# Optimization experiments

Measured on AMD Instinct MI355X. Metric: run time of the kernel, lower is better.

## Reference

```python
import jax, jax.numpy as jnp
import numpy as np

B, M, N = 32, 256, 4000          # images, gt boxes/img, proposals/img
NUM_CLASSES = 80                 # cfg.MODEL.ROI_HEADS.NUM_CLASSES
BATCH_PER_IMG = 512              # cfg.MODEL.ROI_HEADS.BATCH_SIZE_PER_IMAGE
POS_FRAC = 0.25                  # cfg.MODEL.ROI_HEADS.POSITIVE_FRACTION
IOU_THRESH = 0.5                 # cfg.MODEL.ROI_HEADS.IOU_THRESHOLDS
IMG_SIZE = 1024.0


def _make_boxes(key, shape):
    # valid xyxy boxes: centers in [0, IMG_SIZE], sides in [4, 256]
    k1, k2 = jax.random.split(key)
    c = jax.random.uniform(k1, shape[:-1] + (2,)) * IMG_SIZE
    wh = 4.0 + jax.random.uniform(k2, shape[:-1] + (2,)) * 252.0
    return jnp.concatenate([c - wh / 2, c + wh / 2], axis=-1)


def setup_inputs() -> dict:
    key = jax.random.key(0)
    kg, kp, kc, kr = jax.random.split(key, 4)
    gt_boxes = _make_boxes(kg, (B, M, 4))
    proposal_boxes = _make_boxes(kp, (B, N, 4))
    gt_classes = jax.random.randint(kc, (B, M), 0, NUM_CLASSES, dtype=jnp.int32)
    # random priorities stand in for torch.randperm in subsample_labels
    rand_priority = jax.random.uniform(kr, (B, N + M))
    return {"gt_boxes": gt_boxes, "proposal_boxes": proposal_boxes,
            "gt_classes": gt_classes, "rand_priority": rand_priority}


def _pairwise_iou(b1, b2):
    # b1 [M,4], b2 [K,4] -> [M,K]  (detectron2 pairwise_iou)
    a1 = (b1[:, 2] - b1[:, 0]) * (b1[:, 3] - b1[:, 1])
    a2 = (b2[:, 2] - b2[:, 0]) * (b2[:, 3] - b2[:, 1])
    lt = jnp.maximum(b1[:, None, :2], b2[None, :, :2])
    rb = jnp.minimum(b1[:, None, 2:], b2[None, :, 2:])
    wh = jnp.clip(rb - lt, 0.0)
    inter = wh[..., 0] * wh[..., 1]
    union = a1[:, None] + a2[None, :] - inter
    return jnp.where(inter > 0, inter / union, 0.0)


def _rank_desc(score):
    # rank of each element in descending order of score
    order = jnp.argsort(-score)
    return jnp.zeros_like(order).at[order].set(jnp.arange(order.shape[0]))


def _per_image(gt_b, prop_b, gt_c, pri):
    # add_ground_truth_to_proposals (proposal_append_gt=True)
    boxes = jnp.concatenate([prop_b, gt_b], axis=0)          # [N+M, 4]
    iou = _pairwise_iou(gt_b, boxes)                          # [M, N+M]
    # Matcher(thresholds=[0.5], labels=[0,1], allow_low_quality=False)
    matched_idxs = jnp.argmax(iou, axis=0)                    # [N+M]
    matched_vals = jnp.max(iou, axis=0)
    matched_labels = (matched_vals >= IOU_THRESH).astype(jnp.int32)
    # _sample_proposals: assign classes, bg where label==0
    cls = gt_c[matched_idxs]
    cls = jnp.where(matched_labels == 0, NUM_CLASSES, cls)
    # subsample_labels with random priorities (fixed-shape, jit-safe)
    fg = cls < NUM_CLASSES
    bg = cls == NUM_CLASSES
    num_fg = jnp.minimum(fg.sum(), int(BATCH_PER_IMG * POS_FRAC))
    num_bg = jnp.minimum(bg.sum(), BATCH_PER_IMG - num_fg)
    sel_fg = fg & (_rank_desc(jnp.where(fg, pri, -jnp.inf)) < num_fg)
    sel_bg = bg & (_rank_desc(jnp.where(bg, pri, -jnp.inf)) < num_bg)
    sel = sel_fg | sel_bg
    _, idx = jax.lax.top_k(jnp.where(sel, pri, -jnp.inf), BATCH_PER_IMG)
    labels = jnp.where(sel[idx], cls[idx], -1)                # pad -1 if <512 valid
    return iou, matched_idxs, matched_labels, idx, labels


def reference(gt_boxes, proposal_boxes, gt_classes, rand_priority):
    return jax.vmap(_per_image)(gt_boxes, proposal_boxes, gt_classes, rand_priority)
```

## Files before the change

kernel.cpp:

```cpp
#include <hip/hip_runtime.h>
#include <hip/hip_bf16.h>

#define Bimg 32
#define Mgt 256
#define Nprop 4000
#define KBOX (Nprop + Mgt)
#define NCLS 80
#define BATCH 512
#define NFG_CAP 128
#define NBINS 1024
#define BINCAP 1024
#define MT 32
#define MS (Mgt / MT)
#define KCH ((KBOX + 1023) / 1024)

typedef float f32x4 __attribute__((ext_vector_type(4)));

__global__ __launch_bounds__(256) void iou_part_kernel(
    const float* __restrict__ gt_boxes,
    const float* __restrict__ prop_boxes,
    float* __restrict__ out_iou,
    unsigned long long* __restrict__ part)
{
    const int b  = blockIdx.z;
    const int ms = blockIdx.y;
    const int m0 = ms * MT;
    const int k0 = (blockIdx.x * 256 + threadIdx.x) * 4;

    __shared__ float4 gbox[MT];
    __shared__ float  garea[MT];
    if (threadIdx.x < MT) {
        float4 g = ((const float4*)(gt_boxes + (size_t)b * Mgt * 4))[m0 + threadIdx.x];
        gbox[threadIdx.x] = g;
        garea[threadIdx.x] = (g.z - g.x) * (g.w - g.y);
    }
    __syncthreads();
    if (k0 >= KBOX) return;

    float4 bx[4]; float a2[4];
    if (k0 < Nprop) {
        const float4* pp = (const float4*)(prop_boxes + (size_t)b * Nprop * 4);
        #pragma unroll
        for (int c = 0; c < 4; ++c) bx[c] = pp[k0 + c];
    } else {
        const float4* gg = (const float4*)(gt_boxes + (size_t)b * Mgt * 4);
        #pragma unroll
        for (int c = 0; c < 4; ++c) bx[c] = gg[k0 - Nprop + c];
    }
    #pragma unroll
    for (int c = 0; c < 4; ++c) a2[c] = (bx[c].z - bx[c].x) * (bx[c].w - bx[c].y);

    unsigned long long bk[4] = {0ull, 0ull, 0ull, 0ull};
    float* orow = out_iou + (size_t)b * Mgt * KBOX + (size_t)m0 * KBOX + k0;

    for (int mm = 0; mm < MT; ++mm) {
        float4 g = gbox[mm];
        float ga = garea[mm];
        float io[4];
        #pragma unroll
        for (int c = 0; c < 4; ++c) {
            float ltx = fmaxf(g.x, bx[c].x), lty = fmaxf(g.y, bx[c].y);
            float rbx = fminf(g.z, bx[c].z), rby = fminf(g.w, bx[c].w);
            float w = fmaxf(rbx - ltx, 0.0f);
            float h = fmaxf(rby - lty, 0.0f);
            float inter = w * h;
            float uni = ga + a2[c] - inter;
            float iou = (inter > 0.0f) ? (inter / uni) : 0.0f;
            io[c] = iou;
            unsigned long long key =
                ((unsigned long long)__float_as_uint(iou) << 8) |
                (unsigned long long)(255 - (m0 + mm));
            if (key > bk[c]) bk[c] = key;
        }
        f32x4 res = { io[0], io[1], io[2], io[3] };
        __builtin_nontemporal_store(res, (f32x4*)(orow + (size_t)mm * KBOX));
    }

    unsigned long long* pr = part + ((size_t)b * MS + ms) * KBOX + k0;
    *(ulonglong2*)(pr)     = make_ulonglong2(bk[0], bk[1]);
    *(ulonglong2*)(pr + 2) = make_ulonglong2(bk[2], bk[3]);
}

__global__ __launch_bounds__(256) void match_reduce_kernel(
    const unsigned long long* __restrict__ part,
    float* __restrict__ out_midx,
    float* __restrict__ out_mlab)
{
    const int b = blockIdx.y;
    const int k = blockIdx.x * 256 + threadIdx.x;
    if (k >= KBOX) return;
    unsigned long long best = 0ull;
    #pragma unroll
    for (int s = 0; s < MS; ++s) {
        unsigned long long key = part[((size_t)b * MS + s) * KBOX + k];
        if (key > best) best = key;
    }
    float v = __uint_as_float((unsigned)(best >> 8));
    int   m = 255 - (int)(best & 0xFFull);
    out_midx[(size_t)b * KBOX + k] = (float)m;
    out_mlab[(size_t)b * KBOX + k] = (v >= 0.5f) ? 1.0f : 0.0f;
}

__global__ __launch_bounds__(1024) void sample_kernel(
    const int*   __restrict__ gt_classes,
    const float* __restrict__ pri,
    const float* __restrict__ midx,
    const float* __restrict__ mlab,
    float* __restrict__ out_idx,
    float* __restrict__ out_lab)
{
    const int b   = blockIdx.x;
    const int tid = threadIdx.x;

    __shared__ unsigned long long keys[KBOX];
    __shared__ unsigned short     clsS[KBOX];
    __shared__ unsigned char      selA[KBOX];
    __shared__ int histP[NBINS];
    __shared__ int sufP[NBINS];
    __shared__ unsigned long long binFG[BINCAP];
    __shared__ unsigned long long binBG[BINCAP];
    __shared__ unsigned long long selKeys[BATCH];
    __shared__ int cntF, cntB, cntSel, sTF, sTB;

    histP[tid] = 0;
    if (tid == 0) { cntF = 0; cntB = 0; cntSel = 0; sTF = -1; sTB = -1; }
    __syncthreads();

    for (int i = tid; i < KBOX; i += 1024) {
        float p  = pri[(size_t)b * KBOX + i];
        int   mi = (int)midx[(size_t)b * KBOX + i];
        float ml = mlab[(size_t)b * KBOX + i];
        int c = (ml != 0.0f) ? gt_classes[b * Mgt + mi] : NCLS;
        clsS[i] = (unsigned short)c;
        selA[i] = 0;
        unsigned pb = __float_as_uint(p);
        keys[i] = ((unsigned long long)pb << 32) |
                  (unsigned long long)(0xFFFFFFFFu - (unsigned)i);
        int bucket = (int)(p * (float)NBINS);
        bucket = min(max(bucket, 0), NBINS - 1);
        atomicAdd(&histP[bucket], (c < NCLS) ? 1 : (1 << 16));
    }
    __syncthreads();

    sufP[tid] = histP[tid];
    __syncthreads();
    for (int off = 1; off < NBINS; off <<= 1) {
        int v = sufP[tid];
        int add = (tid + off < NBINS) ? sufP[tid + off] : 0;
        __syncthreads();
        sufP[tid] = v + add;
        __syncthreads();
    }
    const int total_fg = sufP[0] & 0xFFFF;
    const int total_bg = (sufP[0] >> 16) & 0xFFFF;
    const int num_fg = min(total_fg, NFG_CAP);
    const int num_bg = min(total_bg, BATCH - num_fg);

    {
        int sf  = sufP[tid] & 0xFFFF;
        int sfn = (tid < NBINS - 1) ? (sufP[tid + 1] & 0xFFFF) : 0;
        if (num_fg > 0 && sf >= num_fg && sfn < num_fg) sTF = tid;
        int sb  = (sufP[tid] >> 16) & 0xFFFF;
        int sbn = (tid < NBINS - 1) ? ((sufP[tid + 1] >> 16) & 0xFFFF) : 0;
        if (num_bg > 0 && sb >= num_bg && sbn < num_bg) sTB = tid;
    }
    __syncthreads();
    const int tF = sTF, tB = sTB;
    const int aboveF = (tF >= 0 && tF < NBINS - 1) ? (sufP[tF + 1] & 0xFFFF) : 0;
    const int aboveB = (tB >= 0 && tB < NBINS - 1) ? ((sufP[tB + 1] >> 16) & 0xFFFF) : 0;
    const int needF = num_fg - aboveF;
    const int needB = num_bg - aboveB;

    for (int i = tid; i < KBOX; i += 1024) {
        unsigned long long key = keys[i];
        float p = __uint_as_float((unsigned)(key >> 32));
        int bucket = (int)(p * (float)NBINS);
        bucket = min(max(bucket, 0), NBINS - 1);
        if (clsS[i] < NCLS) {
            if (tF >= 0) {
                if (bucket > tF) selA[i] = 1;
                else if (bucket == tF) { int j = atomicAdd(&cntF, 1); if (j < BINCAP) binFG[j] = key; }
            }
        } else {
            if (tB >= 0) {
                if (bucket > tB) selA[i] = 1;
                else if (bucket == tB) { int j = atomicAdd(&cntB, 1); if (j < BINCAP) binBG[j] = key; }
            }
        }
    }
    __syncthreads();

    {
        int cf = min(cntF, BINCAP);
        for (int j = tid; j < cf; j += 1024) {
            unsigned long long key = binFG[j];
            int rank = 0;
            for (int l = 0; l < cf; ++l) rank += (binFG[l] > key) ? 1 : 0;
            if (rank < needF) { unsigned kk = 0xFFFFFFFFu - (unsigned)(key & 0xFFFFFFFFull); selA[kk] = 1; }
        }
        int cb = min(cntB, BINCAP);
        for (int j = tid; j < cb; j += 1024) {
            unsigned long long key = binBG[j];
            int rank = 0;
            for (int l = 0; l < cb; ++l) rank += (binBG[l] > key) ? 1 : 0;
            if (rank < needB) { unsigned kk = 0xFFFFFFFFu - (unsigned)(key & 0xFFFFFFFFull); selA[kk] = 1; }
        }
    }
    __syncthreads();

    const int total_sel = num_fg + num_bg;
    if (tid < BATCH && tid >= total_sel) selKeys[tid] = 0ull;
    for (int i = tid; i < KBOX; i += 1024) {
        if (selA[i]) {
            int p = atomicAdd(&cntSel, 1);
            selKeys[p] = keys[i];
        }
    }
    __syncthreads();

    for (int k2 = 2; k2 <= BATCH; k2 <<= 1) {
        for (int j = k2 >> 1; j > 0; j >>= 1) {
            if (tid < BATCH) {
                int i = tid, ixj = i ^ j;
                if (ixj > i) {
                    unsigned long long a = selKeys[i], c2 = selKeys[ixj];
                    bool up = ((i & k2) == 0);
                    if (up ? (a < c2) : (a > c2)) { selKeys[i] = c2; selKeys[ixj] = a; }
                }
            }
            __syncthreads();
        }
    }

    if (tid < BATCH) {
        unsigned long long key = selKeys[tid];
        if (key != 0ull) {
            unsigned kk = 0xFFFFFFFFu - (unsigned)(key & 0xFFFFFFFFull);
            out_idx[b * BATCH + tid] = (float)kk;
            out_lab[b * BATCH + tid] = (float)clsS[kk];
        }
    }

    if (total_sel < BATCH) {
        __syncthreads();
        int loc[5]; int acc = 0;
        #pragma unroll
        for (int q = 0; q < 5; ++q) {
            int i = tid * 5 + q;
            int contrib = (i < KBOX && !selA[i]) ? 1 : 0;
            loc[q] = acc; acc += contrib;
        }
        histP[tid] = acc;
        __syncthreads();
        for (int off = 1; off < 1024; off <<= 1) {
            int v = histP[tid];
            int add = (tid >= off) ? histP[tid - off] : 0;
            __syncthreads();
            histP[tid] = v + add;
            __syncthreads();
        }
        int excl = tid ? histP[tid - 1] : 0;
        #pragma unroll
        for (int q = 0; q < 5; ++q) {
            int i = tid * 5 + q;
            if (i < KBOX && !selA[i]) {
                int p = total_sel + excl + loc[q];
                if (p < BATCH) { out_idx[b * BATCH + p] = (float)i; out_lab[b * BATCH + p] = -1.0f; }
            }
        }
    }
}

extern "C" void kernel_launch(void* const* d_in, const int* in_sizes, int n_in,
                              void* d_out, int out_size, void* d_ws, size_t ws_size,
                              hipStream_t stream) {
    const float* gt_boxes   = (const float*)d_in[0];
    const float* prop_boxes = (const float*)d_in[1];
    const int*   gt_classes = (const int*)d_in[2];
    const float* rand_pri   = (const float*)d_in[3];

    float* out = (float*)d_out;
    const size_t off_iou  = 0;
    const size_t off_midx = (size_t)Bimg * Mgt * KBOX;
    const size_t off_mlab = off_midx + (size_t)Bimg * KBOX;
    const size_t off_idx  = off_mlab + (size_t)Bimg * KBOX;
    const size_t off_lab  = off_idx  + (size_t)Bimg * BATCH;

    unsigned long long* part = (unsigned long long*)d_ws;

    dim3 gridA(KCH, MS, Bimg);
    iou_part_kernel<<<gridA, 256, 0, stream>>>(
        gt_boxes, prop_boxes, out + off_iou, part);

    dim3 gridR((KBOX + 255) / 256, Bimg);
    match_reduce_kernel<<<gridR, 256, 0, stream>>>(
        part, out + off_midx, out + off_mlab);

    sample_kernel<<<Bimg, 1024, 0, stream>>>(
        gt_classes, rand_pri,
        out + off_midx, out + off_mlab,
        out + off_idx, out + off_lab);
}
```

Before: 65.89 us.

## Fuse match reduction via atomicMax, replace bitonic sort with rank scatter, warp-shuffle scan

The separate match-reduce kernel is removed. The IoU kernel now does a global 64-bit atomicMax of packed (iou, gt index) keys into a zeroed buffer, and the sampling kernel decodes matched index and label itself. The GT tile shrinks from 32 to 16 rows, which doubles the grid. The sampling kernel packs the class into the priority key, replaces the suffix-sum loop with wave-shuffle scans, and replaces the 512-element bitonic sort with an O(n^2) rank-and-scatter. The change trades one kernel launch and the partials round trip for a memset and atomic contention.

```diff
diff --git a/kernel.cpp b/kernel.cpp
--- a/kernel.cpp
+++ b/kernel.cpp
@@ -10,17 +10,18 @@
 #define NFG_CAP 128
 #define NBINS 1024
 #define BINCAP 1024
-#define MT 32
+#define MT 16
 #define MS (Mgt / MT)
 #define KCH ((KBOX + 1023) / 1024)
 
 typedef float f32x4 __attribute__((ext_vector_type(4)));
+typedef unsigned long long ull;
 
 __global__ __launch_bounds__(256) void iou_part_kernel(
     const float* __restrict__ gt_boxes,
     const float* __restrict__ prop_boxes,
     float* __restrict__ out_iou,
-    unsigned long long* __restrict__ part)
+    ull* __restrict__ gpart)
 {
     const int b  = blockIdx.z;
     const int ms = blockIdx.y;
@@ -50,7 +51,8 @@
     #pragma unroll
     for (int c = 0; c < 4; ++c) a2[c] = (bx[c].z - bx[c].x) * (bx[c].w - bx[c].y);
 
-    unsigned long long bk[4] = {0ull, 0ull, 0ull, 0ull};
+    float bestv[4] = {-1.f, -1.f, -1.f, -1.f};
+    int   bestm[4] = {0, 0, 0, 0};
     float* orow = out_iou + (size_t)b * Mgt * KBOX + (size_t)m0 * KBOX + k0;
 
     for (int mm = 0; mm < MT; ++mm) {
@@ -67,59 +69,43 @@
             float uni = ga + a2[c] - inter;
             float iou = (inter > 0.0f) ? (inter / uni) : 0.0f;
             io[c] = iou;
-            unsigned long long key =
-                ((unsigned long long)__float_as_uint(iou) << 8) |
-                (unsigned long long)(255 - (m0 + mm));
-            if (key > bk[c]) bk[c] = key;
+            if (iou > bestv[c]) { bestv[c] = iou; bestm[c] = m0 + mm; }
         }
         f32x4 res = { io[0], io[1], io[2], io[3] };
         __builtin_nontemporal_store(res, (f32x4*)(orow + (size_t)mm * KBOX));
     }
 
-    unsigned long long* pr = part + ((size_t)b * MS + ms) * KBOX + k0;
-    *(ulonglong2*)(pr)     = make_ulonglong2(bk[0], bk[1]);
-    *(ulonglong2*)(pr + 2) = make_ulonglong2(bk[2], bk[3]);
-}
-
-__global__ __launch_bounds__(256) void match_reduce_kernel(
-    const unsigned long long* __restrict__ part,
-    float* __restrict__ out_midx,
-    float* __restrict__ out_mlab)
-{
-    const int b = blockIdx.y;
-    const int k = blockIdx.x * 256 + threadIdx.x;
-    if (k >= KBOX) return;
-    unsigned long long best = 0ull;
+    ull* pr = gpart + (size_t)b * KBOX + k0;
     #pragma unroll
-    for (int s = 0; s < MS; ++s) {
-        unsigned long long key = part[((size_t)b * MS + s) * KBOX + k];
-        if (key > best) best = key;
-    }
-    float v = __uint_as_float((unsigned)(best >> 8));
-    int   m = 255 - (int)(best & 0xFFull);
-    out_midx[(size_t)b * KBOX + k] = (float)m;
-    out_mlab[(size_t)b * KBOX + k] = (v >= 0.5f) ? 1.0f : 0.0f;
+    for (int c = 0; c < 4; ++c) {
+        ull key = ((ull)__float_as_uint(bestv[c]) << 8) |
+                  (ull)(255 - bestm[c]);
+        atomicMax(pr + c, key);
+    }
 }
 
 __global__ __launch_bounds__(1024) void sample_kernel(
     const int*   __restrict__ gt_classes,
     const float* __restrict__ pri,
-    const float* __restrict__ midx,
-    const float* __restrict__ mlab,
+    const ull*   __restrict__ gpart,
+    float* __restrict__ out_midx,
+    float* __restrict__ out_mlab,
     float* __restrict__ out_idx,
     float* __restrict__ out_lab)
 {
-    const int b   = blockIdx.x;
-    const int tid = threadIdx.x;
-
-    __shared__ unsigned long long keys[KBOX];
-    __shared__ unsigned short     clsS[KBOX];
-    __shared__ unsigned char      selA[KBOX];
+    const int b    = blockIdx.x;
+    const int tid  = threadIdx.x;
+    const int lane = tid & 63;
+    const int wv   = tid >> 6;
+
+    __shared__ ull keys[KBOX];
+    __shared__ unsigned char selA[KBOX];
     __shared__ int histP[NBINS];
-    __shared__ int sufP[NBINS];
-    __shared__ unsigned long long binFG[BINCAP];
-    __shared__ unsigned long long binBG[BINCAP];
-    __shared__ unsigned long long selKeys[BATCH];
+    __shared__ int sufP[NBINS + 1];
+    __shared__ ull binFG[BINCAP];
+    __shared__ ull binBG[BINCAP];
+    __shared__ __align__(16) ull selKeys[BATCH + 2];
+    __shared__ int waveTot[16], waveOff[16];
     __shared__ int cntF, cntB, cntSel, sTF, sTB;
 
     histP[tid] = 0;
@@ -128,29 +114,46 @@
 
     for (int i = tid; i < KBOX; i += 1024) {
         float p  = pri[(size_t)b * KBOX + i];
-        int   mi = (int)midx[(size_t)b * KBOX + i];
-        float ml = mlab[(size_t)b * KBOX + i];
-        int c = (ml != 0.0f) ? gt_classes[b * Mgt + mi] : NCLS;
-        clsS[i] = (unsigned short)c;
+        ull  bk  = gpart[(size_t)b * KBOX + i];
+        float v  = __uint_as_float((unsigned)(bk >> 8));
+        int   mi = 255 - (int)(bk & 0xFFull);
+        bool  fg = (v >= 0.5f);
+        int  cls = fg ? gt_classes[b * Mgt + mi] : NCLS;
+        out_midx[(size_t)b * KBOX + i] = (float)mi;
+        out_mlab[(size_t)b * KBOX + i] = fg ? 1.0f : 0.0f;
+        unsigned pb = __float_as_uint(p);
+        keys[i] = ((ull)pb << 32) |
+                  ((ull)(0xFFFFu - (unsigned)i) << 16) |
+                  ((ull)(unsigned)cls << 8);
         selA[i] = 0;
-        unsigned pb = __float_as_uint(p);
-        keys[i] = ((unsigned long long)pb << 32) |
-                  (unsigned long long)(0xFFFFFFFFu - (unsigned)i);
         int bucket = (int)(p * (float)NBINS);
         bucket = min(max(bucket, 0), NBINS - 1);
-        atomicAdd(&histP[bucket], (c < NCLS) ? 1 : (1 << 16));
-    }
-    __syncthreads();
-
-    sufP[tid] = histP[tid];
-    __syncthreads();
-    for (int off = 1; off < NBINS; off <<= 1) {
-        int v = sufP[tid];
-        int add = (tid + off < NBINS) ? sufP[tid + off] : 0;
-        __syncthreads();
-        sufP[tid] = v + add;
-        __syncthreads();
-    }
+        atomicAdd(&histP[bucket], fg ? 1 : (1 << 16));
+    }
+    __syncthreads();
+
+    int v = histP[tid];
+    #pragma unroll
+    for (int off = 1; off < 64; off <<= 1) {
+        int o = __shfl_down(v, off);
+        if (lane + off < 64) v += o;
+    }
+    if (lane == 0) waveTot[wv] = v;
+    __syncthreads();
+    if (wv == 0) {
+        int t = (lane < 16) ? waveTot[lane] : 0;
+        #pragma unroll
+        for (int off = 1; off < 64; off <<= 1) {
+            int o = __shfl_down(t, off);
+            if (lane + off < 64) t += o;
+        }
+        if (lane < 16) waveOff[lane] = t - waveTot[lane];
+    }
+    __syncthreads();
+    sufP[tid] = v + waveOff[wv];
+    if (tid == 0) sufP[NBINS] = 0;
+    __syncthreads();
+
     const int total_fg = sufP[0] & 0xFFFF;
     const int total_bg = (sufP[0] >> 16) & 0xFFFF;
     const int num_fg = min(total_fg, NFG_CAP);
@@ -158,25 +161,26 @@
 
     {
         int sf  = sufP[tid] & 0xFFFF;
-        int sfn = (tid < NBINS - 1) ? (sufP[tid + 1] & 0xFFFF) : 0;
+        int sfn = sufP[tid + 1] & 0xFFFF;
         if (num_fg > 0 && sf >= num_fg && sfn < num_fg) sTF = tid;
         int sb  = (sufP[tid] >> 16) & 0xFFFF;
-        int sbn = (tid < NBINS - 1) ? ((sufP[tid + 1] >> 16) & 0xFFFF) : 0;
+        int sbn = (sufP[tid + 1] >> 16) & 0xFFFF;
         if (num_bg > 0 && sb >= num_bg && sbn < num_bg) sTB = tid;
     }
     __syncthreads();
     const int tF = sTF, tB = sTB;
-    const int aboveF = (tF >= 0 && tF < NBINS - 1) ? (sufP[tF + 1] & 0xFFFF) : 0;
-    const int aboveB = (tB >= 0 && tB < NBINS - 1) ? ((sufP[tB + 1] >> 16) & 0xFFFF) : 0;
+    const int aboveF = (tF >= 0) ? (sufP[tF + 1] & 0xFFFF) : 0;
+    const int aboveB = (tB >= 0) ? ((sufP[tB + 1] >> 16) & 0xFFFF) : 0;
     const int needF = num_fg - aboveF;
     const int needB = num_bg - aboveB;
 
     for (int i = tid; i < KBOX; i += 1024) {
-        unsigned long long key = keys[i];
+        ull key = keys[i];
         float p = __uint_as_float((unsigned)(key >> 32));
         int bucket = (int)(p * (float)NBINS);
         bucket = min(max(bucket, 0), NBINS - 1);
-        if (clsS[i] < NCLS) {
+        bool fg = ((unsigned)(key >> 8) & 0xFFu) < NCLS;
+        if (fg) {
             if (tF >= 0) {
                 if (bucket > tF) selA[i] = 1;
                 else if (bucket == tF) { int j = atomicAdd(&cntF, 1); if (j < BINCAP) binFG[j] = key; }
@@ -193,23 +197,21 @@
     {
         int cf = min(cntF, BINCAP);
         for (int j = tid; j < cf; j += 1024) {
-            unsigned long long key = binFG[j];
+            ull key = binFG[j];
             int rank = 0;
             for (int l = 0; l < cf; ++l) rank += (binFG[l] > key) ? 1 : 0;
-            if (rank < needF) { unsigned kk = 0xFFFFFFFFu - (unsigned)(key & 0xFFFFFFFFull); selA[kk] = 1; }
+            if (rank < needF) { unsigned kk = 0xFFFFu - (unsigned)((key >> 16) & 0xFFFFu); selA[kk] = 1; }
         }
         int cb = min(cntB, BINCAP);
         for (int j = tid; j < cb; j += 1024) {
-            unsigned long long key = binBG[j];
+            ull key = binBG[j];
             int rank = 0;
             for (int l = 0; l < cb; ++l) rank += (binBG[l] > key) ? 1 : 0;
-            if (rank < needB) { unsigned kk = 0xFFFFFFFFu - (unsigned)(key & 0xFFFFFFFFull); selA[kk] = 1; }
-        }
-    }
-    __syncthreads();
-
-    const int total_sel = num_fg + num_bg;
-    if (tid < BATCH && tid >= total_sel) selKeys[tid] = 0ull;
+            if (rank < needB) { unsigned kk = 0xFFFFu - (unsigned)((key >> 16) & 0xFFFFu); selA[kk] = 1; }
+        }
+    }
+    __syncthreads();
+
     for (int i = tid; i < KBOX; i += 1024) {
         if (selA[i]) {
             int p = atomicAdd(&cntSel, 1);
@@ -217,31 +219,26 @@
         }
     }
     __syncthreads();
-
-    for (int k2 = 2; k2 <= BATCH; k2 <<= 1) {
-        for (int j = k2 >> 1; j > 0; j >>= 1) {
-            if (tid < BATCH) {
-                int i = tid, ixj = i ^ j;
-                if (ixj > i) {
-                    unsigned long long a = selKeys[i], c2 = selKeys[ixj];
-                    bool up = ((i & k2) == 0);
-                    if (up ? (a < c2) : (a > c2)) { selKeys[i] = c2; selKeys[ixj] = a; }
-                }
-            }
-            __syncthreads();
-        }
-    }
-
-    if (tid < BATCH) {
-        unsigned long long key = selKeys[tid];
-        if (key != 0ull) {
-            unsigned kk = 0xFFFFFFFFu - (unsigned)(key & 0xFFFFFFFFull);
-            out_idx[b * BATCH + tid] = (float)kk;
-            out_lab[b * BATCH + tid] = (float)clsS[kk];
-        }
-    }
-
-    if (total_sel < BATCH) {
+    const int ns = cntSel;
+    if (tid == 0) { selKeys[ns] = 0ull; selKeys[ns + 1] = 0ull; }
+    __syncthreads();
+
+    if (tid < ns) {
+        ull key = selKeys[tid];
+        int rank = 0;
+        const int n2 = (ns + 1) & ~1;
+        for (int l = 0; l < n2; l += 2) {
+            ulonglong2 two = *(const ulonglong2*)&selKeys[l];
+            rank += (two.x > key) ? 1 : 0;
+            rank += (two.y > key) ? 1 : 0;
+        }
+        unsigned kk = 0xFFFFu - (unsigned)((key >> 16) & 0xFFFFu);
+        int cls = (int)((key >> 8) & 0xFFu);
+        out_idx[b * BATCH + rank] = (float)kk;
+        out_lab[b * BATCH + rank] = (float)cls;
+    }
+
+    if (ns < BATCH) {
         __syncthreads();
         int loc[5]; int acc = 0;
         #pragma unroll
@@ -253,10 +250,10 @@
         histP[tid] = acc;
         __syncthreads();
         for (int off = 1; off < 1024; off <<= 1) {
-            int v = histP[tid];
+            int vv = histP[tid];
             int add = (tid >= off) ? histP[tid - off] : 0;
             __syncthreads();
-            histP[tid] = v + add;
+            histP[tid] = vv + add;
             __syncthreads();
         }
         int excl = tid ? histP[tid - 1] : 0;
@@ -264,7 +261,7 @@
         for (int q = 0; q < 5; ++q) {
             int i = tid * 5 + q;
             if (i < KBOX && !selA[i]) {
-                int p = total_sel + excl + loc[q];
+                int p = ns + excl + loc[q];
                 if (p < BATCH) { out_idx[b * BATCH + p] = (float)i; out_lab[b * BATCH + p] = -1.0f; }
             }
         }
@@ -286,18 +283,16 @@
     const size_t off_idx  = off_mlab + (size_t)Bimg * KBOX;
     const size_t off_lab  = off_idx  + (size_t)Bimg * BATCH;
 
-    unsigned long long* part = (unsigned long long*)d_ws;
+    ull* gpart = (ull*)d_ws;
+
+    hipMemsetAsync(gpart, 0, (size_t)Bimg * KBOX * sizeof(ull), stream);
 
     dim3 gridA(KCH, MS, Bimg);
     iou_part_kernel<<<gridA, 256, 0, stream>>>(
-        gt_boxes, prop_boxes, out + off_iou, part);
-
-    dim3 gridR((KBOX + 255) / 256, Bimg);
-    match_reduce_kernel<<<gridR, 256, 0, stream>>>(
-        part, out + off_midx, out + off_mlab);
+        gt_boxes, prop_boxes, out + off_iou, gpart);
 
     sample_kernel<<<Bimg, 1024, 0, stream>>>(
-        gt_classes, rand_pri,
+        gt_classes, rand_pri, gpart,
         out + off_midx, out + off_mlab,
         out + off_idx, out + off_lab);
 }
```

New measurement: 99.61 us. +51.2%, slower.
